# Performance work log

Measured on AMD Instinct MI355X. Metric: run time of the kernel, lower is better.

## Reference

```python
import jax, jax.numpy as jnp
import numpy as np

N, D, C = 131072, 256, 1000
EPS = 1e-6


def setup_inputs() -> dict:
    key = jax.random.key(0)
    k1, k2, k3, k4 = jax.random.split(key, 4)
    feats = jax.random.normal(k1, (N, D), dtype=jnp.float32)
    pseudo_lbls = jax.random.randint(k2, (N,), 0, C)
    src_proto = jax.random.normal(k3, (C, D), dtype=jnp.float32)
    # uniform in [0.5, 1.5) to keep the Mahalanobis denominator well-conditioned
    src_proto_cov = jax.random.uniform(k4, (C, D), dtype=jnp.float32) + 0.5
    return {"feats": feats, "pseudo_lbls": pseudo_lbls,
            "src_proto": src_proto, "src_proto_cov": src_proto_cov}


def reference(feats, pseudo_lbls, src_proto, src_proto_cov):
    # Fused scatter-mean over classes (replaces the python loop over unique labels).
    num_classes, feat_dim = src_proto.shape
    counts = jax.ops.segment_sum(jnp.ones((feats.shape[0],), feats.dtype),
                                 pseudo_lbls, num_segments=num_classes)  # [C]
    sums = jax.ops.segment_sum(feats, pseudo_lbls, num_segments=num_classes)  # [C, D]
    means = sums / jnp.maximum(counts, 1.0)[:, None]                      # [C, D]
    present = counts > 0                                                  # [C]
    # GSSLoss: mean over the [n_uniq, D] elements of (mean - proto)^2 / (cov + eps)
    per_elem = (means - src_proto) ** 2 / (src_proto_cov + EPS)           # [C, D]
    per_elem = jnp.where(present[:, None], per_elem, 0.0)
    n_present = jnp.sum(present.astype(feats.dtype))
    loss = jnp.sum(per_elem) / (n_present * feat_dim)
    return loss
```

## Files before the change

### kernel.cpp

```cpp
#include <hip/hip_runtime.h>

#define EPS 1e-6f
#define CAP 512


__global__ void bucket_kernel(const int* __restrict__ lbls,
                              int* __restrict__ counts,
                              int* __restrict__ rowidx, int n) {
    int i = blockIdx.x * blockDim.x + threadIdx.x;
    if (i < n) {
        int l = lbls[i];
        int pos = atomicAdd(&counts[l], 1);
        if (pos < CAP) rowidx[(size_t)l * CAP + pos] = i;
    }
}

__global__ __launch_bounds__(256)
void partial_kernel(const float* __restrict__ feats,
                    const int* __restrict__ rowidx,
                    const int* __restrict__ counts,
                    float* __restrict__ partials, int d) {
    int blk  = blockIdx.x;
    int c    = blk >> 1;
    int j    = blk & 1;
    int t    = threadIdx.x;
    int wave = t >> 6;
    int col4 = t & 63;
    int stride4 = d >> 2;

    int cnt = counts[c];
    if (cnt > CAP) cnt = CAP;
    int half = (cnt + 1) >> 1;
    int lo = j ? half : 0;
    int hi = j ? cnt : half;
    int m  = hi - lo;

    __shared__ int sidx[(CAP + 1) / 2 + 1];
    for (int i = t; i < m; i += 256)
        sidx[i] = rowidx[(size_t)c * CAP + lo + i];
    __syncthreads();

    const float4* f4 = (const float4*)feats;
    float4 acc = make_float4(0.f, 0.f, 0.f, 0.f);

    int i = wave;
    for (; i + 28 < m; i += 32) {
        int r0 = sidx[i];
        int r1 = sidx[i + 4];
        int r2 = sidx[i + 8];
        int r3 = sidx[i + 12];
        int r4 = sidx[i + 16];
        int r5 = sidx[i + 20];
        int r6 = sidx[i + 24];
        int r7 = sidx[i + 28];
        float4 v0 = f4[(size_t)r0 * stride4 + col4];
        float4 v1 = f4[(size_t)r1 * stride4 + col4];
        float4 v2 = f4[(size_t)r2 * stride4 + col4];
        float4 v3 = f4[(size_t)r3 * stride4 + col4];
        float4 v4 = f4[(size_t)r4 * stride4 + col4];
        float4 v5 = f4[(size_t)r5 * stride4 + col4];
        float4 v6 = f4[(size_t)r6 * stride4 + col4];
        float4 v7 = f4[(size_t)r7 * stride4 + col4];
        acc.x += ((v0.x + v1.x) + (v2.x + v3.x)) + ((v4.x + v5.x) + (v6.x + v7.x));
        acc.y += ((v0.y + v1.y) + (v2.y + v3.y)) + ((v4.y + v5.y) + (v6.y + v7.y));
        acc.z += ((v0.z + v1.z) + (v2.z + v3.z)) + ((v4.z + v5.z) + (v6.z + v7.z));
        acc.w += ((v0.w + v1.w) + (v2.w + v3.w)) + ((v4.w + v5.w) + (v6.w + v7.w));
    }
    for (; i < m; i += 4) {
        int r0 = sidx[i];
        float4 v0 = f4[(size_t)r0 * stride4 + col4];
        acc.x += v0.x; acc.y += v0.y; acc.z += v0.z; acc.w += v0.w;
    }

    __shared__ float4 sacc[256];
    sacc[t] = acc;
    __syncthreads();

    if (t < 64) {
        float4 a0 = sacc[t], a1 = sacc[t + 64], a2 = sacc[t + 128], a3 = sacc[t + 192];
        float4 r;
        r.x = (a0.x + a1.x) + (a2.x + a3.x);
        r.y = (a0.y + a1.y) + (a2.y + a3.y);
        r.z = (a0.z + a1.z) + (a2.z + a3.z);
        r.w = (a0.w + a1.w) + (a2.w + a3.w);
        ((float4*)partials)[(size_t)blk * stride4 + t] = r;
    }
}

__global__ __launch_bounds__(256)
void finalize_kernel(const float* __restrict__ partials,
                     const int* __restrict__ counts,
                     const float* __restrict__ proto,
                     const float* __restrict__ cov,
                     float* __restrict__ loss_acc,
                     float* __restrict__ npres_acc,
                     int* __restrict__ done,
                     float* __restrict__ out, int c_total, int d) {
    int c = blockIdx.x;
    int t = threadIdx.x;
    size_t idx = (size_t)c * d + t;
    float a = partials[(size_t)(2 * c) * d + t] + partials[(size_t)(2 * c + 1) * d + t];
    int cnt = counts[c];
    float present = (cnt > 0) ? 1.0f : 0.0f;
    float mean = a / fmaxf((float)cnt, 1.0f);
    float diff = mean - proto[idx];
    float pe = present * diff * diff / (cov[idx] + EPS);

    for (int off = 32; off > 0; off >>= 1)
        pe += __shfl_down(pe, off, 64);
    __shared__ float s[4];
    if ((t & 63) == 0) s[t >> 6] = pe;
    __syncthreads();
    if (t == 0) {
        atomicAdd(loss_acc, (s[0] + s[1]) + (s[2] + s[3]));
        atomicAdd(npres_acc, present);
        __threadfence();
        int prev = atomicAdd(done, 1);
        if (prev == c_total - 1) {
            float L = atomicAdd(loss_acc, 0.0f);
            float P = atomicAdd(npres_acc, 0.0f);
            out[0] = L / (P * (float)d);
        }
    }
}

extern "C" void kernel_launch(void* const* d_in, const int* in_sizes, int n_in,
                              void* d_out, int out_size, void* d_ws, size_t ws_size,
                              hipStream_t stream) {
    const float* feats = (const float*)d_in[0];
    const int*   lbls  = (const int*)d_in[1];
    const float* proto = (const float*)d_in[2];
    const float* cov   = (const float*)d_in[3];

    int n_rows = in_sizes[1];
    int d      = in_sizes[0] / n_rows;
    int c      = in_sizes[2] / d;

    int*   counts    = (int*)d_ws;
    float* loss_acc  = (float*)d_ws + c;
    float* npres_acc = loss_acc + 1;
    int*   done      = (int*)d_ws + c + 2;
    int*   rowidx    = (int*)d_ws + c + 3;
    float* partials  = (float*)d_ws + c + 3 + (size_t)c * CAP;

    hipMemsetAsync(d_ws, 0, ((size_t)c + 3) * sizeof(int), stream);

    int nb = (n_rows + 255) / 256;
    bucket_kernel<<<nb, 256, 0, stream>>>(lbls, counts, rowidx, n_rows);
    partial_kernel<<<2 * c, 256, 0, stream>>>(feats, rowidx, counts, partials, d);
    finalize_kernel<<<c, 256, 0, stream>>>(partials, counts, proto, cov,
                                           loss_acc, npres_acc, done,
                                           (float*)d_out, c, d);
}
```

Before: 273.6 us.

## Fuse bucket, partial-sum and finalize into one cooperative kernel with grid syncs

Replaces the memset plus three kernel launches with a single cooperative kernel of one block per class. It zeroes the counters, buckets the labels with a grid-stride loop, gathers and sums each class's rows, and computes the Mahalanobis term in place, with grid.sync between phases. This removes launch overhead and the round trip of the partials buffer, but it halves the number of blocks doing the gather (one per class instead of two). It also depends on all 1000 blocks of 256 threads being co-resident, and grid syncs have their own cost.

```diff
diff --git a/kernel.cpp b/kernel.cpp
--- a/kernel.cpp
+++ b/kernel.cpp
@@ -1,50 +1,56 @@
 #include <hip/hip_runtime.h>
+#include <hip/hip_cooperative_groups.h>
+
+namespace cg = cooperative_groups;
 
 #define EPS 1e-6f
 #define CAP 512
 
 
-__global__ void bucket_kernel(const int* __restrict__ lbls,
-                              int* __restrict__ counts,
-                              int* __restrict__ rowidx, int n) {
-    int i = blockIdx.x * blockDim.x + threadIdx.x;
-    if (i < n) {
+__global__ __launch_bounds__(256, 4)
+void fused_kernel(const float* __restrict__ feats,
+                  const int* __restrict__ lbls,
+                  const float* __restrict__ proto,
+                  const float* __restrict__ cov,
+                  int* __restrict__ counts,
+                  int* __restrict__ rowidx,
+                  float* __restrict__ loss_acc,
+                  float* __restrict__ npres_acc,
+                  float* __restrict__ out,
+                  int n, int c, int d) {
+    cg::grid_group grid = cg::this_grid();
+    int t   = threadIdx.x;
+    int b   = blockIdx.x;
+    int gid = b * 256 + t;
+    int nthreads = gridDim.x * 256;
+
+    if (gid < c) counts[gid] = 0;
+    if (gid == 0) { loss_acc[0] = 0.0f; npres_acc[0] = 0.0f; }
+    grid.sync();
+
+    for (int i = gid; i < n; i += nthreads) {
         int l = lbls[i];
         int pos = atomicAdd(&counts[l], 1);
         if (pos < CAP) rowidx[(size_t)l * CAP + pos] = i;
     }
-}
+    grid.sync();
 
-__global__ __launch_bounds__(256)
-void partial_kernel(const float* __restrict__ feats,
-                    const int* __restrict__ rowidx,
-                    const int* __restrict__ counts,
-                    float* __restrict__ partials, int d) {
-    int blk  = blockIdx.x;
-    int c    = blk >> 1;
-    int j    = blk & 1;
-    int t    = threadIdx.x;
     int wave = t >> 6;
     int col4 = t & 63;
     int stride4 = d >> 2;
+    int cnt = counts[b];
+    if (cnt > CAP) cnt = CAP;
 
-    int cnt = counts[c];
-    if (cnt > CAP) cnt = CAP;
-    int half = (cnt + 1) >> 1;
-    int lo = j ? half : 0;
-    int hi = j ? cnt : half;
-    int m  = hi - lo;
-
-    __shared__ int sidx[(CAP + 1) / 2 + 1];
-    for (int i = t; i < m; i += 256)
-        sidx[i] = rowidx[(size_t)c * CAP + lo + i];
+    __shared__ int sidx[CAP];
+    for (int i = t; i < cnt; i += 256)
+        sidx[i] = rowidx[(size_t)b * CAP + i];
     __syncthreads();
 
     const float4* f4 = (const float4*)feats;
     float4 acc = make_float4(0.f, 0.f, 0.f, 0.f);
 
     int i = wave;
-    for (; i + 28 < m; i += 32) {
+    for (; i + 28 < cnt; i += 32) {
         int r0 = sidx[i];
         int r1 = sidx[i + 4];
         int r2 = sidx[i + 8];
@@ -66,7 +72,7 @@
         acc.z += ((v0.z + v1.z) + (v2.z + v3.z)) + ((v4.z + v5.z) + (v6.z + v7.z));
         acc.w += ((v0.w + v1.w) + (v2.w + v3.w)) + ((v4.w + v5.w) + (v6.w + v7.w));
     }
-    for (; i < m; i += 4) {
+    for (; i < cnt; i += 4) {
         int r0 = sidx[i];
         float4 v0 = f4[(size_t)r0 * stride4 + col4];
         acc.x += v0.x; acc.y += v0.y; acc.z += v0.z; acc.w += v0.w;
@@ -78,49 +84,39 @@
 
     if (t < 64) {
         float4 a0 = sacc[t], a1 = sacc[t + 64], a2 = sacc[t + 128], a3 = sacc[t + 192];
-        float4 r;
-        r.x = (a0.x + a1.x) + (a2.x + a3.x);
-        r.y = (a0.y + a1.y) + (a2.y + a3.y);
-        r.z = (a0.z + a1.z) + (a2.z + a3.z);
-        r.w = (a0.w + a1.w) + (a2.w + a3.w);
-        ((float4*)partials)[(size_t)blk * stride4 + t] = r;
+        float sx = (a0.x + a1.x) + (a2.x + a3.x);
+        float sy = (a0.y + a1.y) + (a2.y + a3.y);
+        float sz = (a0.z + a1.z) + (a2.z + a3.z);
+        float sw = (a0.w + a1.w) + (a2.w + a3.w);
+
+        float present = (cnt > 0) ? 1.0f : 0.0f;
+        float inv = 1.0f / fmaxf((float)cnt, 1.0f);
+
+        float4 p = ((const float4*)proto)[(size_t)b * stride4 + t];
+        float4 q = ((const float4*)cov)[(size_t)b * stride4 + t];
+
+        float dx = sx * inv - p.x;
+        float dy = sy * inv - p.y;
+        float dz = sz * inv - p.z;
+        float dw = sw * inv - p.w;
+        float pe = dx * dx / (q.x + EPS) + dy * dy / (q.y + EPS)
+                 + dz * dz / (q.z + EPS) + dw * dw / (q.w + EPS);
+        pe *= present;
+
+        for (int off = 32; off > 0; off >>= 1)
+            pe += __shfl_down(pe, off, 64);
+
+        if (t == 0) {
+            atomicAdd(loss_acc, pe);
+            atomicAdd(npres_acc, present);
+        }
     }
-}
+    grid.sync();
 
-__global__ __launch_bounds__(256)
-void finalize_kernel(const float* __restrict__ partials,
-                     const int* __restrict__ counts,
-                     const float* __restrict__ proto,
-                     const float* __restrict__ cov,
-                     float* __restrict__ loss_acc,
-                     float* __restrict__ npres_acc,
-                     int* __restrict__ done,
-                     float* __restrict__ out, int c_total, int d) {
-    int c = blockIdx.x;
-    int t = threadIdx.x;
-    size_t idx = (size_t)c * d + t;
-    float a = partials[(size_t)(2 * c) * d + t] + partials[(size_t)(2 * c + 1) * d + t];
-    int cnt = counts[c];
-    float present = (cnt > 0) ? 1.0f : 0.0f;
-    float mean = a / fmaxf((float)cnt, 1.0f);
-    float diff = mean - proto[idx];
-    float pe = present * diff * diff / (cov[idx] + EPS);
-
-    for (int off = 32; off > 0; off >>= 1)
-        pe += __shfl_down(pe, off, 64);
-    __shared__ float s[4];
-    if ((t & 63) == 0) s[t >> 6] = pe;
-    __syncthreads();
-    if (t == 0) {
-        atomicAdd(loss_acc, (s[0] + s[1]) + (s[2] + s[3]));
-        atomicAdd(npres_acc, present);
-        __threadfence();
-        int prev = atomicAdd(done, 1);
-        if (prev == c_total - 1) {
-            float L = atomicAdd(loss_acc, 0.0f);
-            float P = atomicAdd(npres_acc, 0.0f);
-            out[0] = L / (P * (float)d);
-        }
+    if (gid == 0) {
+        float L = atomicAdd(loss_acc, 0.0f);
+        float P = atomicAdd(npres_acc, 0.0f);
+        out[0] = L / (P * (float)d);
     }
 }
 
@@ -139,16 +135,14 @@
     int*   counts    = (int*)d_ws;
     float* loss_acc  = (float*)d_ws + c;
     float* npres_acc = loss_acc + 1;
-    int*   done      = (int*)d_ws + c + 2;
-    int*   rowidx    = (int*)d_ws + c + 3;
-    float* partials  = (float*)d_ws + c + 3 + (size_t)c * CAP;
+    int*   rowidx    = (int*)d_ws + c + 2;
+    float* out       = (float*)d_out;
 
-    hipMemsetAsync(d_ws, 0, ((size_t)c + 3) * sizeof(int), stream);
+    void* args[] = { (void*)&feats, (void*)&lbls, (void*)&proto, (void*)&cov,
+                     (void*)&counts, (void*)&rowidx, (void*)&loss_acc,
+                     (void*)&npres_acc, (void*)&out,
+                     (void*)&n_rows, (void*)&c, (void*)&d };
 
-    int nb = (n_rows + 255) / 256;
-    bucket_kernel<<<nb, 256, 0, stream>>>(lbls, counts, rowidx, n_rows);
-    partial_kernel<<<2 * c, 256, 0, stream>>>(feats, rowidx, counts, partials, d);
-    finalize_kernel<<<c, 256, 0, stream>>>(partials, counts, proto, cov,
-                                           loss_acc, npres_acc, done,
-                                           (float*)d_out, c, d);
+    hipLaunchCooperativeKernel((void*)fused_kernel, dim3(c), dim3(256),
+                               args, 0, stream);
 }
```

After: 486.2 us. 1.78x slower.

## Replace bucketed gather with streaming LDS-atomic segment sums per column slice

Applied to the files above, without the earlier changes.

Drops the per-class row-index bucketing and gather. Each block now streams a contiguous row chunk for one 16-column slice and accumulates per-class sums with shared-memory float atomics. Partials are written per chunk and slice, and finalize reduces the 32 chunks. This swaps random row gathers for coalesced streaming and removes the CAP truncation, but each block reads a narrow 64-byte slice per row and relies on LDS atomics, which can contend when labels collide. It also needs about 68KB of LDS per block.

```diff
diff --git a/kernel.cpp b/kernel.cpp
--- a/kernel.cpp
+++ b/kernel.cpp
@@ -1,89 +1,59 @@
 #include <hip/hip_runtime.h>
 
 #define EPS 1e-6f
-#define CAP 512
+#define NCHUNK 32
+#define WSLICE 16
+#define NSLICE 16
+#define LSTRIDE 17
 
 
-__global__ void bucket_kernel(const int* __restrict__ lbls,
-                              int* __restrict__ counts,
-                              int* __restrict__ rowidx, int n) {
+__global__ void hist_kernel(const int* __restrict__ lbls,
+                            int* __restrict__ counts, int n) {
     int i = blockIdx.x * blockDim.x + threadIdx.x;
-    if (i < n) {
-        int l = lbls[i];
-        int pos = atomicAdd(&counts[l], 1);
-        if (pos < CAP) rowidx[(size_t)l * CAP + pos] = i;
-    }
+    if (i < n) atomicAdd(&counts[lbls[i]], 1);
 }
 
 __global__ __launch_bounds__(256)
-void partial_kernel(const float* __restrict__ feats,
-                    const int* __restrict__ rowidx,
-                    const int* __restrict__ counts,
-                    float* __restrict__ partials, int d) {
-    int blk  = blockIdx.x;
-    int c    = blk >> 1;
-    int j    = blk & 1;
-    int t    = threadIdx.x;
-    int wave = t >> 6;
-    int col4 = t & 63;
+void stream_kernel(const float* __restrict__ feats,
+                   const int* __restrict__ lbls,
+                   float* __restrict__ partials,
+                   int n, int c, int d) {
+    extern __shared__ float lsum[];
+    int bid = blockIdx.x;
+    int s = bid & (NSLICE - 1);
+    int k = bid >> 4;
+    int t = threadIdx.x;
+
+    int lds_elems = c * LSTRIDE;
+    for (int i = t; i < lds_elems; i += 256) lsum[i] = 0.0f;
+    __syncthreads();
+
+    int rows = n / NCHUNK;
+    int row0 = k * rows;
+    int rsub = t >> 2;
+    int a    = t & 3;
+
+    const float4* f4 = (const float4*)feats;
     int stride4 = d >> 2;
 
-    int cnt = counts[c];
-    if (cnt > CAP) cnt = CAP;
-    int half = (cnt + 1) >> 1;
-    int lo = j ? half : 0;
-    int hi = j ? cnt : half;
-    int m  = hi - lo;
-
-    __shared__ int sidx[(CAP + 1) / 2 + 1];
-    for (int i = t; i < m; i += 256)
-        sidx[i] = rowidx[(size_t)c * CAP + lo + i];
+#pragma unroll 4
+    for (int it = 0; it < rows / 64; ++it) {
+        int r = row0 + it * 64 + rsub;
+        int lbl = lbls[r];
+        float4 v = f4[(size_t)r * stride4 + s * 4 + a];
+        float* base = &lsum[lbl * LSTRIDE + a * 4];
+        unsafeAtomicAdd(base + 0, v.x);
+        unsafeAtomicAdd(base + 1, v.y);
+        unsafeAtomicAdd(base + 2, v.z);
+        unsafeAtomicAdd(base + 3, v.w);
+    }
     __syncthreads();
 
-    const float4* f4 = (const float4*)feats;
-    float4 acc = make_float4(0.f, 0.f, 0.f, 0.f);
-
-    int i = wave;
-    for (; i + 28 < m; i += 32) {
-        int r0 = sidx[i];
-        int r1 = sidx[i + 4];
-        int r2 = sidx[i + 8];
-        int r3 = sidx[i + 12];
-        int r4 = sidx[i + 16];
-        int r5 = sidx[i + 20];
-        int r6 = sidx[i + 24];
-        int r7 = sidx[i + 28];
-        float4 v0 = f4[(size_t)r0 * stride4 + col4];
-        float4 v1 = f4[(size_t)r1 * stride4 + col4];
-        float4 v2 = f4[(size_t)r2 * stride4 + col4];
-        float4 v3 = f4[(size_t)r3 * stride4 + col4];
-        float4 v4 = f4[(size_t)r4 * stride4 + col4];
-        float4 v5 = f4[(size_t)r5 * stride4 + col4];
-        float4 v6 = f4[(size_t)r6 * stride4 + col4];
-        float4 v7 = f4[(size_t)r7 * stride4 + col4];
-        acc.x += ((v0.x + v1.x) + (v2.x + v3.x)) + ((v4.x + v5.x) + (v6.x + v7.x));
-        acc.y += ((v0.y + v1.y) + (v2.y + v3.y)) + ((v4.y + v5.y) + (v6.y + v7.y));
-        acc.z += ((v0.z + v1.z) + (v2.z + v3.z)) + ((v4.z + v5.z) + (v6.z + v7.z));
-        acc.w += ((v0.w + v1.w) + (v2.w + v3.w)) + ((v4.w + v5.w) + (v6.w + v7.w));
-    }
-    for (; i < m; i += 4) {
-        int r0 = sidx[i];
-        float4 v0 = f4[(size_t)r0 * stride4 + col4];
-        acc.x += v0.x; acc.y += v0.y; acc.z += v0.z; acc.w += v0.w;
-    }
-
-    __shared__ float4 sacc[256];
-    sacc[t] = acc;
-    __syncthreads();
-
-    if (t < 64) {
-        float4 a0 = sacc[t], a1 = sacc[t + 64], a2 = sacc[t + 128], a3 = sacc[t + 192];
-        float4 r;
-        r.x = (a0.x + a1.x) + (a2.x + a3.x);
-        r.y = (a0.y + a1.y) + (a2.y + a3.y);
-        r.z = (a0.z + a1.z) + (a2.z + a3.z);
-        r.w = (a0.w + a1.w) + (a2.w + a3.w);
-        ((float4*)partials)[(size_t)blk * stride4 + t] = r;
+    float* dst = partials + (size_t)(k * NSLICE + s) * c * WSLICE;
+    int tot = c * WSLICE;
+    for (int i = t; i < tot; i += 256) {
+        int cc = i >> 4, col = i & 15;
+        dst[i] = lsum[cc * LSTRIDE + col];
     }
 }
 
@@ -98,21 +68,27 @@
                      float* __restrict__ out, int c_total, int d) {
     int c = blockIdx.x;
     int t = threadIdx.x;
-    size_t idx = (size_t)c * d + t;
-    float a = partials[(size_t)(2 * c) * d + t] + partials[(size_t)(2 * c + 1) * d + t];
+    int s = t >> 4, col = t & 15;
+
+    float a = 0.0f;
+    for (int k = 0; k < NCHUNK; ++k)
+        a += partials[(size_t)(k * NSLICE + s) * c_total * WSLICE
+                      + (size_t)c * WSLICE + col];
+
     int cnt = counts[c];
     float present = (cnt > 0) ? 1.0f : 0.0f;
     float mean = a / fmaxf((float)cnt, 1.0f);
+    size_t idx = (size_t)c * d + t;
     float diff = mean - proto[idx];
     float pe = present * diff * diff / (cov[idx] + EPS);
 
     for (int off = 32; off > 0; off >>= 1)
         pe += __shfl_down(pe, off, 64);
-    __shared__ float s[4];
-    if ((t & 63) == 0) s[t >> 6] = pe;
+    __shared__ float sred[4];
+    if ((t & 63) == 0) sred[t >> 6] = pe;
     __syncthreads();
     if (t == 0) {
-        atomicAdd(loss_acc, (s[0] + s[1]) + (s[2] + s[3]));
+        atomicAdd(loss_acc, (sred[0] + sred[1]) + (sred[2] + sred[3]));
         atomicAdd(npres_acc, present);
         __threadfence();
         int prev = atomicAdd(done, 1);
@@ -140,14 +116,17 @@
     float* loss_acc  = (float*)d_ws + c;
     float* npres_acc = loss_acc + 1;
     int*   done      = (int*)d_ws + c + 2;
-    int*   rowidx    = (int*)d_ws + c + 3;
-    float* partials  = (float*)d_ws + c + 3 + (size_t)c * CAP;
+    float* partials  = (float*)d_ws + c + 3;
 
     hipMemsetAsync(d_ws, 0, ((size_t)c + 3) * sizeof(int), stream);
 
     int nb = (n_rows + 255) / 256;
-    bucket_kernel<<<nb, 256, 0, stream>>>(lbls, counts, rowidx, n_rows);
-    partial_kernel<<<2 * c, 256, 0, stream>>>(feats, rowidx, counts, partials, d);
+    hist_kernel<<<nb, 256, 0, stream>>>(lbls, counts, n_rows);
+
+    size_t lds_bytes = (size_t)c * LSTRIDE * sizeof(float);
+    stream_kernel<<<NCHUNK * NSLICE, 256, lds_bytes, stream>>>(
+        feats, lbls, partials, n_rows, c, d);
+
     finalize_kernel<<<c, 256, 0, stream>>>(partials, counts, proto, cov,
                                            loss_acc, npres_acc, done,
                                            (float*)d_out, c, d);
```

Result: slower. 401.7 us (+46.8%).
